# Kernel optimization log

Measured on AMD Instinct MI355X. Metric: run time of the kernel, lower is better.

Reference implementation:

```python
import jax, jax.numpy as jnp
import numpy as np

B, W, IN, H, Z, D, OUT, K = 256, 128, 128, 1024, 128, 1024, 128, 3


def _gru_cell(h, x, Wih, Whh, bih, bhh):
    # torch nn.GRU single-layer cell, gate order (r, z, n)
    gi = x @ Wih.T + bih
    gh = h @ Whh.T + bhh
    ir, iz, inn = jnp.split(gi, 3, axis=-1)
    hr, hz, hn = jnp.split(gh, 3, axis=-1)
    r = jax.nn.sigmoid(ir + hr)
    u = jax.nn.sigmoid(iz + hz)
    n = jnp.tanh(inn + r * hn)
    return (1.0 - u) * n + u * h


def setup_inputs():
    key = jax.random.key(0)
    ks = iter(jax.random.split(key, 40))

    def w(shape, fanin):
        return jax.random.normal(next(ks), shape, jnp.float32) / np.float32(np.sqrt(fanin))

    return dict(
        x=jax.random.normal(next(ks), (B, W, IN), jnp.float32),
        eps_q=jax.random.uniform(next(ks), (B, W, Z), jnp.float32),
        eps_p=jax.random.uniform(next(ks), (B, W, OUT), jnp.float32),
        Wih_q=w((3 * H, IN), IN), Whh_q=w((3 * H, H), H),
        bih_q=jnp.zeros(3 * H, jnp.float32), bhh_q=jnp.zeros(3 * H, jnp.float32),
        Wd_q=w((D, Z + H), Z + H), bd_q=jnp.zeros(D, jnp.float32),
        Wmu_q=w((Z, D), D), bmu_q=jnp.zeros(Z, jnp.float32),
        Wsig_q=w((Z, D), D), bsig_q=jnp.zeros(Z, jnp.float32),
        Wp=w((K, Z, Z), Z), bp=jnp.zeros((K, Z), jnp.float32),
        up=0.1 * jax.random.normal(next(ks), (K,), jnp.float32),
        Wlg=w((Z, Z), Z), blg=jnp.zeros(Z, jnp.float32),
        Wih_p=w((3 * H, Z), Z), Whh_p=w((3 * H, H), H),
        bih_p=jnp.zeros(3 * H, jnp.float32), bhh_p=jnp.zeros(3 * H, jnp.float32),
        Wd_p=w((D, H), H), bd_p=jnp.zeros(D, jnp.float32),
        Wmu_p=w((OUT, D), D), bmu_p=jnp.zeros(OUT, jnp.float32),
        Wsig_p=w((OUT, D), D), bsig_p=jnp.zeros(OUT, jnp.float32),
    )


def _forward(x, eps_q, eps_p, Wih_q, Whh_q, bih_q, bhh_q, Wd_q, bd_q, Wmu_q, bmu_q,
             Wsig_q, bsig_q, Wp, bp, up, Wlg, blg, Wih_p, Whh_p, bih_p, bhh_p,
             Wd_p, bd_p, Wmu_p, bmu_p, Wsig_p, bsig_p):
    Bsz = x.shape[0]

    # ---- Qnet: sequential encoder with planar flows ----
    def q_step(carry, inp):
        e, z_prev = carry
        x_t, eps_t = inp  # [B,IN], [B,Z]
        e = _gru_cell(e, x_t, Wih_q, Whh_q, bih_q, bhh_q)
        d = jnp.concatenate([z_prev, e], axis=-1) @ Wd_q.T + bd_q
        mu = d @ Wmu_q.T + bmu_q
        logvar = jax.nn.softplus(d @ Wsig_q.T + bsig_q)
        z = mu + jnp.exp(0.5 * logvar) * eps_t
        for k in range(K):  # planar normalizing flows: z + u * tanh(Wz + b)
            z = z + up[k] * jnp.tanh(z @ Wp[k].T + bp[k])
        return (e, z), (z, mu, logvar)

    e0 = jnp.zeros((Bsz, H), x.dtype)
    z0 = jnp.zeros((Bsz, Z), x.dtype)
    _, (z_seq, mu_seq, lv_seq) = jax.lax.scan(
        q_step, (e0, z0), (jnp.swapaxes(x, 0, 1), jnp.swapaxes(eps_q, 0, 1)))

    # ---- Pnet: sequential decoder ----
    def p_step(d_t, inp):
        z_t, eps_t = inp
        zt = z_t @ Wlg.T + blg  # LGSSM linear
        d_t = _gru_cell(d_t, zt, Wih_p, Whh_p, bih_p, bhh_p)
        dd = d_t @ Wd_p.T + bd_p
        mu = dd @ Wmu_p.T + bmu_p
        sigma = jax.nn.softplus(dd @ Wsig_p.T + bsig_p)
        return d_t, mu + sigma * eps_t

    d0 = jnp.zeros((Bsz, H), x.dtype)
    _, out_seq = jax.lax.scan(p_step, d0, (z_seq, jnp.swapaxes(eps_p, 0, 1)))

    return (jnp.swapaxes(out_seq, 0, 1),
            jnp.swapaxes(mu_seq, 0, 1),
            jnp.swapaxes(lv_seq, 0, 1))


def reference(x, eps_q, eps_p, Wih_q, Whh_q, bih_q, bhh_q, Wd_q, bd_q, Wmu_q, bmu_q,
              Wsig_q, bsig_q, Wp, bp, up, Wlg, blg, Wih_p, Whh_p, bih_p, bhh_p,
              Wd_p, bd_p, Wmu_p, bmu_p, Wsig_p, bsig_p):
    return _forward(x, eps_q, eps_p, Wih_q, Whh_q, bih_q, bhh_q, Wd_q, bd_q, Wmu_q,
                    bmu_q, Wsig_q, bsig_q, Wp, bp, up, Wlg, blg, Wih_p, Whh_p,
                    bih_p, bhh_p, Wd_p, bd_p, Wmu_p, bmu_p, Wsig_p, bsig_p)
```

## Files before the change

kernel.cpp:

```cpp
#include <hip/hip_runtime.h>


typedef __bf16 bf16;
typedef __bf16 bf16x8 __attribute__((ext_vector_type(8)));
typedef float  f32x4  __attribute__((ext_vector_type(4)));
typedef unsigned u32;

static constexpr int CB   = 256;
static constexpr int CW   = 128;
static constexpr int CIN  = 128;
static constexpr int CH   = 1024;
static constexpr int CZ   = 128;
static constexpr int CD   = 1024;
static constexpr int COUT = 128;

static constexpr int APITCH     = 1160;
static constexpr int ABUF_BYTES = 16 * APITCH * 2;
static constexpr int REDN       = 8 * 16 * 17;
static constexpr int RED2_BYTES = 2 * REDN * 4;
static constexpr int FLOW_BYTES = (2 * CZ + 2 * 2 * CZ) * 4;
static constexpr int SMEM_BYTES = ABUF_BYTES + RED2_BYTES + FLOW_BYTES;

static constexpr int XCC_GETREG = 20 | (31 << 11);

#define DEV static __device__ __forceinline__

DEV float sigmoidf_(float x) { return 1.0f / (1.0f + expf(-x)); }
DEV float softplusf_(float x) { return x > 20.0f ? x : log1pf(expf(x)); }
DEV bf16x8 ldfrag(const bf16* p) { return *reinterpret_cast<const bf16x8*>(p); }

#define MFMA(a, b, c) __builtin_amdgcn_mfma_f32_16x16x32_bf16((a), (b), (c), 0, 0, 0)

template <bool FAST> DEV bf16x8 ldx16(const bf16* p) {
    bf16x8 v;
    if constexpr (FAST)
        asm volatile("global_load_dwordx4 %0, %1, off sc0\n\ts_waitcnt vmcnt(0)"
                     : "=v"(v) : "v"(p) : "memory");
    else
        asm volatile("global_load_dwordx4 %0, %1, off sc0 sc1\n\ts_waitcnt vmcnt(0)"
                     : "=v"(v) : "v"(p) : "memory");
    return v;
}
template <bool FAST> DEV u32 ldx4(const void* p) {
    u32 v;
    if constexpr (FAST)
        asm volatile("global_load_dword %0, %1, off sc0\n\ts_waitcnt vmcnt(0)"
                     : "=v"(v) : "v"(p) : "memory");
    else
        asm volatile("global_load_dword %0, %1, off sc0 sc1\n\ts_waitcnt vmcnt(0)"
                     : "=v"(v) : "v"(p) : "memory");
    return v;
}
template <bool FAST> DEV void stx4(void* p, u32 v) {
    if constexpr (FAST)
        asm volatile("global_store_dword %0, %1, off sc0" :: "v"(p), "v"(v) : "memory");
    else
        asm volatile("global_store_dword %0, %1, off sc0 sc1" :: "v"(p), "v"(v) : "memory");
}
DEV u32 pk2(float a, float b) {
    union { bf16 h[2]; u32 u; } r;
    r.h[0] = (bf16)a; r.h[1] = (bf16)b;
    return r.u;
}

struct Prm {
    const float *eps_q, *eps_p;
    const float *bih_q, *bhh_q, *bd_q, *bmu_q, *bsig_q;
    const float *Wp, *bp, *up, *Wlg, *blg;
    const float *bih_p, *bhh_p, *bd_p, *bmu_p, *bsig_p;
    const bf16 *x_b, *Wih_qb, *Whh_qb, *Wd_qb, *Wmu_qb, *Wsg_qb;
    const bf16 *Wih_pb, *Whh_pb, *Wd_pb, *Wmu_pb, *Wsg_pb;
    float *e_f0, *e_f1, *d_f0, *d_f1;
    bf16 *e_b0, *e_b1, *d_b0, *d_b1;
    float *ztmp_f;
    bf16 *dvec_b, *ddvec_b;
    bf16 *zflow;
    bf16 *ztlg;
    u32 *qbar, *pbar;
    u32 *zbar, *pdone;
    u32 *xcc, *cnt;
    float *out_o, *out_mu, *out_lv;
};

DEV void gbar_g(u32* flg, int slice, u32 k)
{
    asm volatile("s_waitcnt vmcnt(0)" ::: "memory");
    __syncthreads();
    if (threadIdx.x == 0)
        __hip_atomic_store(&flg[slice * 16], k, __ATOMIC_RELAXED, __HIP_MEMORY_SCOPE_AGENT);
    if (threadIdx.x < 8) {
        while (__hip_atomic_load(&flg[threadIdx.x * 16], __ATOMIC_RELAXED,
                                 __HIP_MEMORY_SCOPE_AGENT) < k)
            __builtin_amdgcn_s_sleep(1);
    }
    __syncthreads();
}

__global__ void k_cvt(const float* __restrict__ src, bf16* __restrict__ dst, int n)
{
    int i = (blockIdx.x * blockDim.x + threadIdx.x) * 4;
    if (i < n) {
        float4 v = *reinterpret_cast<const float4*>(src + i);
        *reinterpret_cast<u32*>(dst + i)     = pk2(v.x, v.y);
        *reinterpret_cast<u32*>(dst + i + 2) = pk2(v.z, v.w);
    }
}

template <bool FAST, int HMODE>
DEV void stage_act(bf16* abuf, int tid, int r0,
                   const bf16* head, long hs, int K1,
                   const bf16* body, long bs)
{
    const int CHN = (K1 + CH) >> 3;
    const int TOT = 16 * CHN;
    for (int idx = tid; idx < TOT; idx += 512) {
        const int row = idx / CHN;
        const int k = (idx - row * CHN) * 8;
        bf16x8 v;
        if (k < K1) {
            const bf16* s = head + (long)(r0 + row) * hs + k;
            if constexpr (HMODE == 0)      v = ldfrag(s);
            else if constexpr (HMODE == 1) v = ldx16<FAST>(s);
            else                           v = ldx16<false>(s);
        } else {
            v = ldx16<FAST>(body + (long)(r0 + row) * bs + (k - K1));
        }
        *reinterpret_cast<bf16x8*>(abuf + (long)row * APITCH + k) = v;
    }
    __syncthreads();
}

template <bool FAST>
DEV void gru_compute(const bf16* abuf, int r0, int n0, int lane, int wave,
                     const bf16* __restrict__ Wih, const bf16* __restrict__ Whh,
                     const float* __restrict__ bih, const float* __restrict__ bhh,
                     const float* __restrict__ Efin,
                     float* __restrict__ Efo, bf16* __restrict__ Ebo)
{
    const int lr = lane & 15, lkE = (lane >> 4) * 8;
    const int c = n0 + wave * 16 + lr;
    const bf16* arow = abuf + (long)lr * APITCH;

    f32x4 acc[4] = {};
#pragma unroll 4
    for (int k = 0; k < CIN; k += 32) {
        bf16x8 a = *reinterpret_cast<const bf16x8*>(arow + k + lkE);
#pragma unroll
        for (int g = 0; g < 3; ++g) {
            bf16x8 b = ldfrag(Wih + ((long)g * CH + c) * CIN + k + lkE);
            const int grp = (g == 2) ? 2 : g;
            acc[grp] = MFMA(a, b, acc[grp]);
        }
    }
#pragma unroll 4
    for (int k = 0; k < CH; k += 32) {
        bf16x8 a = *reinterpret_cast<const bf16x8*>(arow + CIN + k + lkE);
#pragma unroll
        for (int g = 0; g < 3; ++g) {
            bf16x8 b = ldfrag(Whh + ((long)g * CH + c) * CH + k + lkE);
            const int grp = (g == 2) ? 3 : g;
            acc[grp] = MFMA(a, b, acc[grp]);
        }
    }

    const float b0r = bih[c] + bhh[c];
    const float b0z = bih[CH + c] + bhh[CH + c];
    const float bin = bih[2 * CH + c];
    const float bhn = bhh[2 * CH + c];
    const int rbase = r0 + (lane >> 4) * 4;
#pragma unroll
    for (int i = 0; i < 4; ++i) {
        const int row = rbase + i;
        float r = sigmoidf_(acc[0][i] + b0r);
        float u = sigmoidf_(acc[1][i] + b0z);
        float n = tanhf(acc[2][i] + bin + r * (acc[3][i] + bhn));
        float en = (1.0f - u) * n + u * Efin[(long)row * CH + c];
        Efo[(long)row * CH + c] = en;
        float vB = __shfl_xor(en, 1);
        if (!(lane & 1))
            stx4<FAST>(Ebo + (long)row * CH + c, pk2(en, vB));
    }
}

template <bool FAST>
DEV void lin_compute(const bf16* abuf, int r0, int n0, int lane, int wave, int Ktot,
                     const bf16* __restrict__ W,
                     const float* __restrict__ bias, bf16* __restrict__ Out)
{
    const int lr = lane & 15, lkE = (lane >> 4) * 8;
    const int c = n0 + wave * 16 + lr;
    const bf16* arow = abuf + (long)lr * APITCH;
    const bf16* wrow = W + (long)c * Ktot;

    f32x4 acc = {};
#pragma unroll 4
    for (int k = 0; k < CH; k += 32) {
        bf16x8 a = *reinterpret_cast<const bf16x8*>(arow + (Ktot - CH) + k + lkE);
        bf16x8 b = ldfrag(wrow + (Ktot - CH) + k + lkE);
        acc = MFMA(a, b, acc);
    }
    if (Ktot > CH) {
#pragma unroll 4
        for (int k = 0; k < CZ; k += 32) {
            bf16x8 a = *reinterpret_cast<const bf16x8*>(arow + k + lkE);
            bf16x8 b = ldfrag(wrow + k + lkE);
            acc = MFMA(a, b, acc);
        }
    }

    const float bb = bias[c];
    const int rbase = r0 + (lane >> 4) * 4;
#pragma unroll
    for (int i = 0; i < 4; ++i) {
        float v = acc[i] + bb;
        float vB = __shfl_xor(v, 1);
        if (!(lane & 1))
            stx4<FAST>(Out + (long)(rbase + i) * CD + c, pk2(v, vB));
    }
}

template <bool FAST, int MODE>
DEV void phase_tail2(const Prm& p, int t, int slab, int slice, int tid,
                     int lane, int wave, float* Ra, float* Rs,
                     const bf16* __restrict__ A,
                     const bf16* __restrict__ Wa, const bf16* __restrict__ Wb,
                     const float* __restrict__ ba, const float* __restrict__ bb)
{
    const int lr = lane & 15, lkE = (lane >> 4) * 8;
    const int mb = slab * 16;
    const int nb = slice * 16;
    f32x4 am = {}, as = {};
    const int k0 = wave * 128;
#pragma unroll
    for (int kk = 0; kk < 128; kk += 32) {
        const int k = k0 + kk;
        bf16x8 a  = ldx16<FAST>(A + (long)(mb + lr) * CD + k + lkE);
        bf16x8 bm = ldfrag(Wa + (long)(nb + lr) * CD + k + lkE);
        bf16x8 bs = ldfrag(Wb + (long)(nb + lr) * CD + k + lkE);
        am = MFMA(a, bm, am);
        as = MFMA(a, bs, as);
    }
    __syncthreads();
#pragma unroll
    for (int i = 0; i < 4; ++i) {
        Ra[(wave * 16 + (lane >> 4) * 4 + i) * 17 + lr] = am[i];
        Rs[(wave * 16 + (lane >> 4) * 4 + i) * 17 + lr] = as[i];
    }
    __syncthreads();
    if (tid < 256) {
        const int trow = tid >> 4, tcol = tid & 15;
        float vm = 0.f, vs = 0.f;
#pragma unroll
        for (int w = 0; w < 8; ++w) {
            vm += Ra[(w * 16 + trow) * 17 + tcol];
            vs += Rs[(w * 16 + trow) * 17 + tcol];
        }
        const int row = mb + trow, col = nb + tcol;
        if constexpr (MODE == 0) {
            float mu = vm + ba[col];
            float lv = softplusf_(vs + bb[col]);
            float e  = p.eps_q[(long)row * CW * CZ + (long)t * CZ + col];
            float z  = mu + expf(0.5f * lv) * e;
            p.out_mu[(long)row * CW * CZ + (long)t * CZ + col] = mu;
            p.out_lv[(long)row * CW * CZ + (long)t * CZ + col] = lv;
            stx4<FAST>(p.ztmp_f + (long)row * CZ + col, __float_as_uint(z));
        } else {
            float m  = vm + ba[col];
            float sg = softplusf_(vs + bb[col]);
            float e  = p.eps_p[(long)row * CW * COUT + (long)t * COUT + col];
            p.out_o[(long)row * CW * COUT + (long)t * COUT + col] = m + sg * e;
        }
    }
}

template <bool FAST>
DEV void phase_flows2(const Prm& p, int rowbase, int tid, int t, float* zl, float* ps)
{
    const int rg = tid >> 8;
    const int sub = tid & 255;
    const int c = sub & 127, half = sub >> 7;
    const int row = rowbase + rg;
    float* zrow = zl + rg * CZ;
    float* pall = ps + rg * 2 * CZ;

    if (half == 0)
        zrow[c] = __uint_as_float(ldx4<FAST>(p.ztmp_f + (long)row * CZ + c));
    __syncthreads();

#pragma unroll 1
    for (int kf = 0; kf < 3; ++kf) {
        const float* wr = p.Wp + ((long)kf * CZ + c) * CZ + half * 64;
        const float* zh = zrow + half * 64;
        float s = 0.f;
#pragma unroll
        for (int j = 0; j < 64; j += 4) {
            float4 w = *reinterpret_cast<const float4*>(wr + j);
            s += zh[j] * w.x + zh[j + 1] * w.y + zh[j + 2] * w.z + zh[j + 3] * w.w;
        }
        pall[half * CZ + c] = s;
        __syncthreads();
        if (half == 0) {
            float sf = pall[c] + pall[CZ + c] + p.bp[kf * CZ + c];
            zrow[c] += p.up[kf] * tanhf(sf);
        }
        __syncthreads();
    }
    {
        const float* wr = p.Wlg + (long)c * CZ + half * 64;
        const float* zh = zrow + half * 64;
        float s = 0.f;
#pragma unroll
        for (int j = 0; j < 64; j += 4) {
            float4 w = *reinterpret_cast<const float4*>(wr + j);
            s += zh[j] * w.x + zh[j + 1] * w.y + zh[j + 2] * w.z + zh[j + 3] * w.w;
        }
        pall[half * CZ + c] = s;
        __syncthreads();
        if (half == 0) {
            float zt = pall[c] + pall[CZ + c] + p.blg[c];
            float ztB = __shfl_xor(zt, 1);
            if (!(c & 1)) {
                stx4<false>(p.ztlg + ((size_t)(t & 1) * CB + row) * CZ + c, pk2(zt, ztB));
                stx4<FAST>(p.zflow + ((size_t)((t + 1) & 1) * CB + row) * CZ + c,
                           pk2(zrow[c], zrow[c + 1]));
            }
        }
    }
}

template <bool FAST>
DEV void run_q(const Prm& p, int slab, int slice, int tid,
               bf16* abuf, float* Ra, float* Rs, float* ZLp, float* PSp)
{
    const int lane = tid & 63, wave = tid >> 6;
    const int r0 = slab * 16, n0 = slice * 128;
    u32* qb = p.qbar + slab * 8 * 16;
    u32 bk = 0;
#pragma unroll 1
    for (int t = 0; t < CW; ++t) {
        const int bi = t & 1;
        const bf16*  eb_i = bi ? p.e_b1 : p.e_b0;
        const float* ef_i = bi ? p.e_f1 : p.e_f0;
        bf16*  eb_o = bi ? p.e_b0 : p.e_b1;
        float* ef_o = bi ? p.e_f0 : p.e_f1;

        stage_act<FAST, 0>(abuf, tid, r0, p.x_b + (long)t * CIN, (long)CW * CIN,
                           CIN, eb_i, CH);
        gru_compute<FAST>(abuf, r0, n0, lane, wave, p.Wih_qb, p.Whh_qb,
                          p.bih_q, p.bhh_q, ef_i, ef_o, eb_o);
        gbar_g(qb, slice, ++bk);
        stage_act<FAST, 1>(abuf, tid, r0, p.zflow + (size_t)bi * CB * CZ,
                           CZ, CZ, eb_o, CH);
        lin_compute<FAST>(abuf, r0, n0, lane, wave, CZ + CH, p.Wd_qb, p.bd_q, p.dvec_b);
        gbar_g(qb, slice, ++bk);
        phase_tail2<FAST, 0>(p, t, slab, slice, tid, lane, wave, Ra, Rs,
                             p.dvec_b, p.Wmu_qb, p.Wsg_qb, p.bmu_q, p.bsig_q);
        gbar_g(qb, slice, ++bk);
        if (t >= 2) {
            if (tid == 0) {
                while ((int)__hip_atomic_load(&p.pdone[slab * 16], __ATOMIC_RELAXED,
                                              __HIP_MEMORY_SCOPE_AGENT) < t - 1)
                    __builtin_amdgcn_s_sleep(2);
            }
            __syncthreads();
        }
        phase_flows2<FAST>(p, slab * 16 + slice * 2, tid, t, ZLp, PSp);
        gbar_g(qb, slice, ++bk);
        if (slice == 0 && tid == 0)
            __hip_atomic_store(&p.zbar[slab * 16], (u32)(t + 1),
                               __ATOMIC_RELAXED, __HIP_MEMORY_SCOPE_AGENT);
    }
}

template <bool FAST>
DEV void run_p(const Prm& p, int slab, int slice, int tid,
               bf16* abuf, float* Ra, float* Rs)
{
    const int lane = tid & 63, wave = tid >> 6;
    const int r0 = slab * 16, n0 = slice * 128;
    u32* pb = p.pbar + slab * 8 * 16;
    u32 bk = 0;
#pragma unroll 1
    for (int t = 0; t < CW; ++t) {
        if (tid == 0) {
            while (__hip_atomic_load(&p.zbar[slab * 16], __ATOMIC_RELAXED,
                                     __HIP_MEMORY_SCOPE_AGENT) < (u32)(t + 1))
                __builtin_amdgcn_s_sleep(2);
        }
        __syncthreads();

        const int bi = t & 1;
        const bf16*  db_i = bi ? p.d_b1 : p.d_b0;
        const float* df_i = bi ? p.d_f1 : p.d_f0;
        bf16*  db_o = bi ? p.d_b0 : p.d_b1;
        float* df_o = bi ? p.d_f0 : p.d_f1;

        stage_act<FAST, 2>(abuf, tid, r0, p.ztlg + (size_t)bi * CB * CZ,
                           CZ, CZ, db_i, CH);
        gru_compute<FAST>(abuf, r0, n0, lane, wave, p.Wih_pb, p.Whh_pb,
                          p.bih_p, p.bhh_p, df_i, df_o, db_o);
        gbar_g(pb, slice, ++bk);
        if (slice == 0 && tid == 0)
            __hip_atomic_store(&p.pdone[slab * 16], (u32)(t + 1),
                               __ATOMIC_RELAXED, __HIP_MEMORY_SCOPE_AGENT);
        stage_act<FAST, 0>(abuf, tid, r0, nullptr, 0, 0, db_o, CH);
        lin_compute<FAST>(abuf, r0, n0, lane, wave, CH, p.Wd_pb, p.bd_p, p.ddvec_b);
        gbar_g(pb, slice, ++bk);
        phase_tail2<FAST, 1>(p, t, slab, slice, tid, lane, wave, Ra, Rs,
                             p.ddvec_b, p.Wmu_pb, p.Wsg_pb, p.bmu_p, p.bsig_p);
    }
}

__launch_bounds__(512)
__global__ void mega(Prm p)
{
    extern __shared__ char smem[];
    bf16*  abuf = (bf16*)smem;
    float* Ra   = (float*)(smem + ABUF_BYTES);
    float* Rs   = Ra + REDN;
    float* ZLp  = (float*)(smem + ABUF_BYTES + RED2_BYTES);
    float* PSp  = ZLp + 2 * CZ;
    __shared__ int s_fast;

    const int wg = blockIdx.x, tid = threadIdx.x;
    const int gid = wg & 7, m = wg >> 3;
    const bool isQ = gid < 4;
    const int slab = (isQ ? gid : gid - 4) * 4 + (m >> 3);
    const int slice = m & 7;

    const u32 myx = (u32)__builtin_amdgcn_s_getreg(XCC_GETREG);
    if (tid == 0) {
        __hip_atomic_store(&p.xcc[wg * 16], myx, __ATOMIC_RELAXED, __HIP_MEMORY_SCOPE_AGENT);
        __hip_atomic_fetch_add(p.cnt, 1u, __ATOMIC_RELAXED, __HIP_MEMORY_SCOPE_AGENT);
        while (__hip_atomic_load(p.cnt, __ATOMIC_RELAXED, __HIP_MEMORY_SCOPE_AGENT) < 256u)
            __builtin_amdgcn_s_sleep(2);
    }
    __syncthreads();
    if (tid < 64) {
        bool eq = true;
        if (tid < 32) {
            u32 o = __hip_atomic_load(&p.xcc[(gid + 8 * tid) * 16],
                                      __ATOMIC_RELAXED, __HIP_MEMORY_SCOPE_AGENT);
            eq = (o == myx);
        }
        unsigned long long b = __ballot(eq);
        if (tid == 0) s_fast = (b == ~0ull) ? 1 : 0;
    }
    __syncthreads();
    const bool fast = (s_fast != 0);

    if (isQ) {
        if (fast) run_q<true>(p, slab, slice, tid, abuf, Ra, Rs, ZLp, PSp);
        else      run_q<false>(p, slab, slice, tid, abuf, Ra, Rs, ZLp, PSp);
    } else {
        if (fast) run_p<true>(p, slab, slice, tid, abuf, Ra, Rs);
        else      run_p<false>(p, slab, slice, tid, abuf, Ra, Rs);
    }
}

extern "C" void kernel_launch(void* const* d_in, const int* in_sizes, int n_in,
                              void* d_out, int out_size, void* d_ws, size_t ws_size,
                              hipStream_t stream)
{
    Prm p;
    const float* x      = (const float*)d_in[0];
    p.eps_q  = (const float*)d_in[1];
    p.eps_p  = (const float*)d_in[2];
    const float* Wih_q  = (const float*)d_in[3];
    const float* Whh_q  = (const float*)d_in[4];
    p.bih_q  = (const float*)d_in[5];
    p.bhh_q  = (const float*)d_in[6];
    const float* Wd_q   = (const float*)d_in[7];
    p.bd_q   = (const float*)d_in[8];
    const float* Wmu_q  = (const float*)d_in[9];
    p.bmu_q  = (const float*)d_in[10];
    const float* Wsig_q = (const float*)d_in[11];
    p.bsig_q = (const float*)d_in[12];
    p.Wp     = (const float*)d_in[13];
    p.bp     = (const float*)d_in[14];
    p.up     = (const float*)d_in[15];
    p.Wlg    = (const float*)d_in[16];
    p.blg    = (const float*)d_in[17];
    const float* Wih_p  = (const float*)d_in[18];
    const float* Whh_p  = (const float*)d_in[19];
    p.bih_p  = (const float*)d_in[20];
    p.bhh_p  = (const float*)d_in[21];
    const float* Wd_p   = (const float*)d_in[22];
    p.bd_p   = (const float*)d_in[23];
    const float* Wmu_p  = (const float*)d_in[24];
    p.bmu_p  = (const float*)d_in[25];
    const float* Wsig_p = (const float*)d_in[26];
    p.bsig_p = (const float*)d_in[27];

    p.out_o  = (float*)d_out;
    p.out_mu = p.out_o + (size_t)CB * CW * COUT;
    p.out_lv = p.out_mu + (size_t)CB * CW * CZ;

    char* wp_ = (char*)d_ws;
    auto carve = [&](size_t bytes) -> void* {
        void* q = (void*)wp_;
        wp_ += (bytes + 255) & ~(size_t)255;
        return q;
    };
    p.e_f0 = (float*)carve((size_t)CB * CH * 4);
    p.e_f1 = (float*)carve((size_t)CB * CH * 4);
    p.d_f0 = (float*)carve((size_t)CB * CH * 4);
    p.d_f1 = (float*)carve((size_t)CB * CH * 4);
    p.e_b0 = (bf16*)carve((size_t)CB * CH * 2);
    p.e_b1 = (bf16*)carve((size_t)CB * CH * 2);
    p.d_b0 = (bf16*)carve((size_t)CB * CH * 2);
    p.d_b1 = (bf16*)carve((size_t)CB * CH * 2);
    p.ztmp_f  = (float*)carve((size_t)CB * CZ * 4);
    p.dvec_b  = (bf16*)carve((size_t)CB * CD * 2);
    p.ddvec_b = (bf16*)carve((size_t)CB * CD * 2);
    p.zflow   = (bf16*)carve((size_t)2 * CB * CZ * 2);
    p.ztlg    = (bf16*)carve((size_t)2 * CB * CZ * 2);
    p.qbar    = (u32*)carve((size_t)16 * 8 * 16 * 4);
    p.pbar    = (u32*)carve((size_t)16 * 8 * 16 * 4);
    p.zbar    = (u32*)carve((size_t)16 * 16 * 4);
    p.pdone   = (u32*)carve((size_t)16 * 16 * 4);
    p.xcc     = (u32*)carve((size_t)256 * 16 * 4);
    p.cnt     = (u32*)carve(256);
    bf16* x_b    = (bf16*)carve((size_t)CB * CW * CIN * 2);
    bf16* Wih_qb = (bf16*)carve((size_t)3 * CH * CIN * 2);
    bf16* Whh_qb = (bf16*)carve((size_t)3 * CH * CH * 2);
    bf16* Wd_qb  = (bf16*)carve((size_t)CD * (CZ + CH) * 2);
    bf16* Wmu_qb = (bf16*)carve((size_t)CZ * CD * 2);
    bf16* Wsg_qb = (bf16*)carve((size_t)CZ * CD * 2);
    bf16* Wih_pb = (bf16*)carve((size_t)3 * CH * CZ * 2);
    bf16* Whh_pb = (bf16*)carve((size_t)3 * CH * CH * 2);
    bf16* Wd_pb  = (bf16*)carve((size_t)CD * CH * 2);
    bf16* Wmu_pb = (bf16*)carve((size_t)COUT * CD * 2);
    bf16* Wsg_pb = (bf16*)carve((size_t)COUT * CD * 2);
    p.x_b = x_b;       p.Wih_qb = Wih_qb; p.Whh_qb = Whh_qb;
    p.Wd_qb = Wd_qb;   p.Wmu_qb = Wmu_qb; p.Wsg_qb = Wsg_qb;
    p.Wih_pb = Wih_pb; p.Whh_pb = Whh_pb; p.Wd_pb = Wd_pb;
    p.Wmu_pb = Wmu_pb; p.Wsg_pb = Wsg_pb;

    hipMemsetAsync(p.e_f0, 0, (size_t)CB * CH * 4, stream);
    hipMemsetAsync(p.d_f0, 0, (size_t)CB * CH * 4, stream);
    hipMemsetAsync(p.e_b0, 0, (size_t)CB * CH * 2, stream);
    hipMemsetAsync(p.d_b0, 0, (size_t)CB * CH * 2, stream);
    hipMemsetAsync(p.zflow, 0, (size_t)CB * CZ * 2, stream);
    hipMemsetAsync(p.qbar, 0, (size_t)16 * 8 * 16 * 4, stream);
    hipMemsetAsync(p.pbar, 0, (size_t)16 * 8 * 16 * 4, stream);
    hipMemsetAsync(p.zbar, 0, (size_t)16 * 16 * 4, stream);
    hipMemsetAsync(p.pdone, 0, (size_t)16 * 16 * 4, stream);
    hipMemsetAsync(p.xcc, 0, (size_t)256 * 16 * 4, stream);
    hipMemsetAsync(p.cnt, 0, 256, stream);

    auto cvt = [&](const float* s, bf16* d, size_t n) {
        k_cvt<<<dim3((unsigned)((n / 4 + 255) / 256)), dim3(256), 0, stream>>>(s, d, (int)n);
    };
    cvt(x,      x_b,    (size_t)CB * CW * CIN);
    cvt(Wih_q,  Wih_qb, (size_t)3 * CH * CIN);
    cvt(Whh_q,  Whh_qb, (size_t)3 * CH * CH);
    cvt(Wd_q,   Wd_qb,  (size_t)CD * (CZ + CH));
    cvt(Wmu_q,  Wmu_qb, (size_t)CZ * CD);
    cvt(Wsig_q, Wsg_qb, (size_t)CZ * CD);
    cvt(Wih_p,  Wih_pb, (size_t)3 * CH * CZ);
    cvt(Whh_p,  Whh_pb, (size_t)3 * CH * CH);
    cvt(Wd_p,   Wd_pb,  (size_t)CD * CH);
    cvt(Wmu_p,  Wmu_pb, (size_t)COUT * CD);
    cvt(Wsig_p, Wsg_pb, (size_t)COUT * CD);

    mega<<<dim3(256), dim3(512), SMEM_BYTES, stream>>>(p);
}
```

Before: 8.709 ms.

## Batch global loads and software-pipeline weight prefetch in GRU and linear GEMMs

Replaces per-load waitcnt inline-asm loads in activation staging and the tail GEMM with non-waiting loads issued together and a single vmcnt(0) wait. This lets many memory requests be in flight at once instead of serializing each. In the GRU and linear compute loops, weight fragments are now prefetched into a rotating register ring several k-steps ahead, so MFMAs overlap with weight fetches. The trade-offs are higher register pressure and a staging loop that now assumes the body width is exactly CH with 512 threads.

```diff
diff --git a/kernel.cpp b/kernel.cpp
--- a/kernel.cpp
+++ b/kernel.cpp
@@ -50,6 +50,20 @@
         asm volatile("global_load_dword %0, %1, off sc0 sc1\n\ts_waitcnt vmcnt(0)"
                      : "=v"(v) : "v"(p) : "memory");
     return v;
+}
+template <bool FAST> DEV bf16x8 ldx16_nw(const bf16* p) {
+    bf16x8 v;
+    if constexpr (FAST)
+        asm volatile("global_load_dwordx4 %0, %1, off sc0"
+                     : "=v"(v) : "v"(p) : "memory");
+    else
+        asm volatile("global_load_dwordx4 %0, %1, off sc0 sc1"
+                     : "=v"(v) : "v"(p) : "memory");
+    return v;
+}
+DEV void vm_wait0() {
+    asm volatile("s_waitcnt vmcnt(0)" ::: "memory");
+    __builtin_amdgcn_sched_barrier(0);
 }
 template <bool FAST> DEV void stx4(void* p, u32 v) {
     if constexpr (FAST)
@@ -111,21 +125,32 @@
                    const bf16* head, long hs, int K1,
                    const bf16* body, long bs)
 {
-    const int CHN = (K1 + CH) >> 3;
-    const int TOT = 16 * CHN;
-    for (int idx = tid; idx < TOT; idx += 512) {
-        const int row = idx / CHN;
-        const int k = (idx - row * CHN) * 8;
-        bf16x8 v;
-        if (k < K1) {
+    bf16x8 v[4];
+    long dst[4];
+#pragma unroll
+    for (int j = 0; j < 4; ++j) {
+        const int idx = tid + j * 512;
+        const int row = idx >> 7;
+        const int k = (idx & 127) * 8;
+        v[j] = ldx16_nw<FAST>(body + (long)(r0 + row) * bs + k);
+        dst[j] = (long)row * APITCH + K1 + k;
+    }
+    vm_wait0();
+#pragma unroll
+    for (int j = 0; j < 4; ++j)
+        *reinterpret_cast<bf16x8*>(abuf + dst[j]) = v[j];
+    if (K1 > 0) {
+        const int HC = K1 >> 3;
+        for (int idx = tid; idx < 16 * HC; idx += 512) {
+            const int row = idx / HC;
+            const int k = (idx - row * HC) * 8;
             const bf16* s = head + (long)(r0 + row) * hs + k;
-            if constexpr (HMODE == 0)      v = ldfrag(s);
-            else if constexpr (HMODE == 1) v = ldx16<FAST>(s);
-            else                           v = ldx16<false>(s);
-        } else {
-            v = ldx16<FAST>(body + (long)(r0 + row) * bs + (k - K1));
-        }
-        *reinterpret_cast<bf16x8*>(abuf + (long)row * APITCH + k) = v;
+            bf16x8 hv;
+            if constexpr (HMODE == 0)      hv = ldfrag(s);
+            else if constexpr (HMODE == 1) hv = ldx16<FAST>(s);
+            else                           hv = ldx16<false>(s);
+            *reinterpret_cast<bf16x8*>(abuf + (long)row * APITCH + k) = hv;
+        }
     }
     __syncthreads();
 }
@@ -142,24 +167,45 @@
     const bf16* arow = abuf + (long)lr * APITCH;
 
     f32x4 acc[4] = {};
-#pragma unroll 4
-    for (int k = 0; k < CIN; k += 32) {
-        bf16x8 a = *reinterpret_cast<const bf16x8*>(arow + k + lkE);
-#pragma unroll
-        for (int g = 0; g < 3; ++g) {
-            bf16x8 b = ldfrag(Wih + ((long)g * CH + c) * CIN + k + lkE);
-            const int grp = (g == 2) ? 2 : g;
-            acc[grp] = MFMA(a, b, acc[grp]);
-        }
-    }
-#pragma unroll 4
-    for (int k = 0; k < CH; k += 32) {
-        bf16x8 a = *reinterpret_cast<const bf16x8*>(arow + CIN + k + lkE);
-#pragma unroll
-        for (int g = 0; g < 3; ++g) {
-            bf16x8 b = ldfrag(Whh + ((long)g * CH + c) * CH + k + lkE);
-            const int grp = (g == 2) ? 3 : g;
-            acc[grp] = MFMA(a, b, acc[grp]);
+
+    {
+        bf16x8 wv[4][3];
+#pragma unroll
+        for (int j = 0; j < 4; ++j)
+#pragma unroll
+            for (int g = 0; g < 3; ++g)
+                wv[j][g] = ldfrag(Wih + ((long)g * CH + c) * CIN + j * 32 + lkE);
+#pragma unroll
+        for (int j = 0; j < 4; ++j) {
+            bf16x8 a = *reinterpret_cast<const bf16x8*>(arow + j * 32 + lkE);
+            acc[0] = MFMA(a, wv[j][0], acc[0]);
+            acc[1] = MFMA(a, wv[j][1], acc[1]);
+            acc[2] = MFMA(a, wv[j][2], acc[2]);
+        }
+    }
+    {
+        const bf16* wp0 = Whh + ((long)0 * CH + c) * CH + lkE;
+        const bf16* wp1 = Whh + ((long)1 * CH + c) * CH + lkE;
+        const bf16* wp2 = Whh + ((long)2 * CH + c) * CH + lkE;
+        bf16x8 wv[4][3];
+#pragma unroll
+        for (int j = 0; j < 4; ++j) {
+            wv[j][0] = ldfrag(wp0 + j * 32);
+            wv[j][1] = ldfrag(wp1 + j * 32);
+            wv[j][2] = ldfrag(wp2 + j * 32);
+        }
+#pragma unroll
+        for (int kb = 0; kb < 32; ++kb) {
+            const int sl = kb & 3;
+            bf16x8 a = *reinterpret_cast<const bf16x8*>(arow + CIN + kb * 32 + lkE);
+            acc[0] = MFMA(a, wv[sl][0], acc[0]);
+            acc[1] = MFMA(a, wv[sl][1], acc[1]);
+            acc[3] = MFMA(a, wv[sl][2], acc[3]);
+            if (kb < 28) {
+                wv[sl][0] = ldfrag(wp0 + (kb + 4) * 32);
+                wv[sl][1] = ldfrag(wp1 + (kb + 4) * 32);
+                wv[sl][2] = ldfrag(wp2 + (kb + 4) * 32);
+            }
         }
     }
 
@@ -191,20 +237,30 @@
     const int c = n0 + wave * 16 + lr;
     const bf16* arow = abuf + (long)lr * APITCH;
     const bf16* wrow = W + (long)c * Ktot;
+    const int kofs = Ktot - CH;
 
     f32x4 acc = {};
-#pragma unroll 4
-    for (int k = 0; k < CH; k += 32) {
-        bf16x8 a = *reinterpret_cast<const bf16x8*>(arow + (Ktot - CH) + k + lkE);
-        bf16x8 b = ldfrag(wrow + (Ktot - CH) + k + lkE);
-        acc = MFMA(a, b, acc);
+    {
+        const bf16* wp = wrow + kofs + lkE;
+        bf16x8 wv[8];
+#pragma unroll
+        for (int j = 0; j < 8; ++j) wv[j] = ldfrag(wp + j * 32);
+#pragma unroll
+        for (int kb = 0; kb < 32; ++kb) {
+            const int sl = kb & 7;
+            bf16x8 a = *reinterpret_cast<const bf16x8*>(arow + kofs + kb * 32 + lkE);
+            acc = MFMA(a, wv[sl], acc);
+            if (kb < 24) wv[sl] = ldfrag(wp + (kb + 8) * 32);
+        }
     }
     if (Ktot > CH) {
-#pragma unroll 4
-        for (int k = 0; k < CZ; k += 32) {
-            bf16x8 a = *reinterpret_cast<const bf16x8*>(arow + k + lkE);
-            bf16x8 b = ldfrag(wrow + k + lkE);
-            acc = MFMA(a, b, acc);
+        bf16x8 wv[4];
+#pragma unroll
+        for (int j = 0; j < 4; ++j) wv[j] = ldfrag(wrow + j * 32 + lkE);
+#pragma unroll
+        for (int j = 0; j < 4; ++j) {
+            bf16x8 a = *reinterpret_cast<const bf16x8*>(arow + j * 32 + lkE);
+            acc = MFMA(a, wv[j], acc);
         }
     }
 
@@ -231,14 +287,19 @@
     const int nb = slice * 16;
     f32x4 am = {}, as = {};
     const int k0 = wave * 128;
-#pragma unroll
-    for (int kk = 0; kk < 128; kk += 32) {
-        const int k = k0 + kk;
-        bf16x8 a  = ldx16<FAST>(A + (long)(mb + lr) * CD + k + lkE);
-        bf16x8 bm = ldfrag(Wa + (long)(nb + lr) * CD + k + lkE);
-        bf16x8 bs = ldfrag(Wb + (long)(nb + lr) * CD + k + lkE);
-        am = MFMA(a, bm, am);
-        as = MFMA(a, bs, as);
+    bf16x8 av[4], bmv[4], bsv[4];
+#pragma unroll
+    for (int j = 0; j < 4; ++j) {
+        const int k = k0 + j * 32;
+        av[j]  = ldx16_nw<FAST>(A + (long)(mb + lr) * CD + k + lkE);
+        bmv[j] = ldfrag(Wa + (long)(nb + lr) * CD + k + lkE);
+        bsv[j] = ldfrag(Wb + (long)(nb + lr) * CD + k + lkE);
+    }
+    vm_wait0();
+#pragma unroll
+    for (int j = 0; j < 4; ++j) {
+        am = MFMA(av[j], bmv[j], am);
+        as = MFMA(av[j], bsv[j], as);
     }
     __syncthreads();
 #pragma unroll
```

After: 8.089 ms. 7.1% less time.
